# Kernel tuning notes

Measured on AMD Instinct MI355X. Metric: run time of the kernel, lower is better.

Reference implementation:

```python
import jax, jax.numpy as jnp
import numpy as np

D_MODEL, N_HEADS, WINDOW, N_STATE = 1024, 16, 256, 128
B, T = 2, 2048
EPS = 1e-5


def _layernorm(x, g, b):
    mu = jnp.mean(x, axis=-1, keepdims=True)
    var = jnp.mean((x - mu) ** 2, axis=-1, keepdims=True)
    return (x - mu) * jax.lax.rsqrt(var + EPS) * g + b


def setup_inputs() -> dict:
    key = jax.random.key(0)
    ks = jax.random.split(key, 20)
    d, h = D_MODEL, 4 * D_MODEL
    s = lambda k, *shape: jax.random.normal(k, shape, jnp.float32) * 0.02
    return {
        "x": jax.random.normal(ks[0], (B, T, d), jnp.float32),
        "ssm_state": jnp.zeros((B, N_STATE), jnp.float32),
        "ln1_g": jnp.ones((d,), jnp.float32), "ln1_b": jnp.zeros((d,), jnp.float32),
        "wq": s(ks[1], d, d), "bq": jnp.zeros((d,), jnp.float32),
        "wk": s(ks[2], d, d), "bk": jnp.zeros((d,), jnp.float32),
        "wv": s(ks[3], d, d), "bv": jnp.zeros((d,), jnp.float32),
        "wo": s(ks[4], d, d), "bo": jnp.zeros((d,), jnp.float32),
        "wg": s(ks[5], d, d), "bg": jnp.zeros((d,), jnp.float32),
        "A": jax.random.uniform(ks[6], (N_STATE,), jnp.float32, -0.1, 0.1),
        "Bw": s(ks[7], d, N_STATE),
        "Cw": s(ks[8], N_STATE, d),
        "ln2_g": jnp.ones((d,), jnp.float32), "ln2_b": jnp.zeros((d,), jnp.float32),
        "w1": s(ks[9], d, h), "b1": jnp.zeros((h,), jnp.float32),
        "w2": s(ks[10], h, d), "b2": jnp.zeros((d,), jnp.float32),
    }


def _forward(x, ssm_state, ln1_g, ln1_b, wq, bq, wk, bk, wv, bv, wo, bo,
             wg, bg, A, Bw, Cw, ln2_g, ln2_b, w1, b1, w2, b2):
    Bsz, Tlen, d = x.shape
    d_h = d // N_HEADS
    xn = _layernorm(x, ln1_g, ln1_b)

    # --- windowed causal attention (dense, per original) ---
    def heads(y):
        return y.reshape(Bsz, Tlen, N_HEADS, d_h).transpose(0, 2, 1, 3)
    Q = heads(xn @ wq + bq)
    K = heads(xn @ wk + bk)
    V = heads(xn @ wv + bv)
    scores = jnp.einsum("bhqd,bhkd->bhqk", Q, K) / (d_h ** 0.5)
    i = jnp.arange(Tlen)[:, None]
    j = jnp.arange(Tlen)[None, :]
    allowed = (j <= i) & (i - j < WINDOW)
    scores = jnp.where(allowed, scores, -jnp.inf)
    attn = jax.nn.softmax(scores, axis=-1)
    ao = jnp.einsum("bhqk,bhkd->bhqd", attn, V)
    ao = ao.transpose(0, 2, 1, 3).reshape(Bsz, Tlen, d)
    attn_out = ao @ wo + bo

    # --- diagonal SSM scan ---
    u = xn @ Bw  # (B,T,N)
    def step(s, u_t):
        s = A * s + u_t
        return s, s
    new_state, states = jax.lax.scan(step, ssm_state, u.transpose(1, 0, 2))
    ssm_out = states.transpose(1, 0, 2) @ Cw  # (B,T,d)

    # --- gated fusion + residual + MLP ---
    g = jax.nn.sigmoid(xn @ wg + bg)
    x = x + g * attn_out + (1.0 - g) * ssm_out
    xn2 = _layernorm(x, ln2_g, ln2_b)
    mlp = jax.nn.gelu(xn2 @ w1 + b1, approximate=False) @ w2 + b2
    return x + mlp, new_state


def reference(x, ssm_state, ln1_g, ln1_b, wq, bq, wk, bk, wv, bv, wo, bo,
              wg, bg, A, Bw, Cw, ln2_g, ln2_b, w1, b1, w2, b2):
    return _forward(x, ssm_state, ln1_g, ln1_b, wq, bq, wk, bk, wv, bv, wo, bo,
                    wg, bg, A, Bw, Cw, ln2_g, ln2_b, w1, b1, w2, b2)
```

## Files before the change

### kernel.cpp

```cpp
#include <hip/hip_runtime.h>

typedef __attribute__((ext_vector_type(8))) short bf16x8;
typedef __attribute__((ext_vector_type(4))) float f32x4;

#define D_MODEL 1024
#define T_LEN 2048
#define BATCH 2
#define N_HEADS 16
#define D_HEAD 64
#define WINDOW 256
#define N_STATE 128
#define D_FF 4096
#define N_CAT 4224
#define LDQ 4352
#define M_ROWS 4096

static __device__ __forceinline__ float bf2f(unsigned short u) {
  union { unsigned int i; float f; } v; v.i = ((unsigned int)u) << 16; return v.f;
}
static __device__ __forceinline__ unsigned short f2bf(float f) {
  unsigned int x = __float_as_uint(f);
  return (unsigned short)((x + 0x7FFFu + ((x >> 16) & 1u)) >> 16);
}

static __device__ __forceinline__ void gl_lds16(const void* g, void* l) {
  __builtin_amdgcn_global_load_lds(
      (const __attribute__((address_space(1))) unsigned int*)g,
      (__attribute__((address_space(3))) unsigned int*)l, 16, 0, 0);
}

__global__ __launch_bounds__(256) void prep_kernel(
    const float* __restrict__ wq, const float* __restrict__ wk,
    const float* __restrict__ wv, const float* __restrict__ wg,
    const float* __restrict__ wo, const float* __restrict__ Bw,
    const float* __restrict__ Cw, const float* __restrict__ w1,
    const float* __restrict__ w2,
    const float* __restrict__ bq, const float* __restrict__ bk,
    const float* __restrict__ bv, const float* __restrict__ bg,
    unsigned short* __restrict__ WcatT, unsigned short* __restrict__ woT,
    unsigned short* __restrict__ CwT, unsigned short* __restrict__ w1T,
    unsigned short* __restrict__ w2T, float* __restrict__ bcat)
{
  const int bid = blockIdx.x;
  if (bid >= 13568) {
    const int i = (bid - 13568) * 256 + threadIdx.x;
    if (i < LDQ) {
      float v = 0.0f;
      if (i < 1024)      v = bq[i];
      else if (i < 2048) v = bk[i - 1024];
      else if (i < 3072) v = bv[i - 2048];
      else if (i < 4096) v = bg[i - 3072];
      bcat[i] = v;
    }
    return;
  }
  const float* src; unsigned short* dst;
  int N, n_off, ldd, x, y;
  if (bid < 5120) {
    const int z = bid >> 10, t = bid & 1023;
    x = t & 31; y = t >> 5;
    src = (z == 0) ? wq : (z == 1) ? wk : (z == 2) ? wv : (z == 3) ? wg : wo;
    dst = (z < 4) ? WcatT : woT;
    n_off = (z < 4) ? z * 1024 : 0;
    N = 1024; ldd = 1024;
  } else if (bid < 5248) {
    const int t = bid - 5120; x = t & 31; y = t >> 5;
    src = Bw; dst = WcatT; n_off = 4096; N = 128; ldd = 1024;
  } else if (bid < 5376) {
    const int t = bid - 5248; x = t & 3; y = t >> 2;
    src = Cw; dst = CwT; n_off = 0; N = 1024; ldd = 128;
  } else if (bid < 9472) {
    const int t = bid - 5376; x = t & 31; y = t >> 5;
    src = w1; dst = w1T; n_off = 0; N = 4096; ldd = 1024;
  } else {
    const int t = bid - 9472; x = t & 127; y = t >> 7;
    src = w2; dst = w2T; n_off = 0; N = 1024; ldd = 4096;
  }
  __shared__ float tile[32][33];
  const int kt = x * 32, nt = y * 32;
  const int c = threadIdx.x & 31, r0 = threadIdx.x >> 5;
#pragma unroll
  for (int i = 0; i < 4; i++) {
    const int r = r0 + i * 8;
    tile[r][c] = src[(size_t)(kt + r) * N + nt + c];
  }
  __syncthreads();
#pragma unroll
  for (int i = 0; i < 4; i++) {
    const int r = r0 + i * 8;
    dst[(size_t)(n_off + nt + r) * ldd + kt + c] = f2bf(tile[c][r]);
  }
}

__global__ __launch_bounds__(256) void vtrans_kernel(
    const unsigned short* __restrict__ qkvgu, unsigned short* __restrict__ VT)
{
  __shared__ unsigned short tile[32][33];
  const int bh = blockIdx.z;
  const int b = bh >> 4, h = bh & 15;
  const int t0 = blockIdx.x * 32, d0 = blockIdx.y * 32;
  const int c = threadIdx.x & 31, r0 = threadIdx.x >> 5;
#pragma unroll
  for (int i = 0; i < 4; i++) {
    const int r = r0 + i * 8;
    tile[r][c] = qkvgu[((size_t)b * T_LEN + t0 + r) * LDQ + 2048 + h * 64 + d0 + c];
  }
  __syncthreads();
#pragma unroll
  for (int i = 0; i < 4; i++) {
    const int r = r0 + i * 8;
    VT[((size_t)bh * 64 + d0 + r) * T_LEN + t0 + c] = tile[c][r];
  }
}

__global__ __launch_bounds__(256) void ln_kernel(
    const float* __restrict__ x, const float* __restrict__ g,
    const float* __restrict__ b, unsigned short* __restrict__ out)
{
  const int row = blockIdx.x, tid = threadIdx.x;
  const float4 xv = ((const float4*)(x + (size_t)row * 1024))[tid];
  float s  = xv.x + xv.y + xv.z + xv.w;
  float s2 = xv.x * xv.x + xv.y * xv.y + xv.z * xv.z + xv.w * xv.w;
#pragma unroll
  for (int off = 32; off >= 1; off >>= 1) {
    s  += __shfl_down(s, off);
    s2 += __shfl_down(s2, off);
  }
  __shared__ float red[8];
  const int wave = tid >> 6;
  if ((tid & 63) == 0) { red[wave] = s; red[4 + wave] = s2; }
  __syncthreads();
  s  = red[0] + red[1] + red[2] + red[3];
  s2 = red[4] + red[5] + red[6] + red[7];
  const float mu = s * (1.0f / 1024.0f);
  const float rs = rsqrtf(s2 * (1.0f / 1024.0f) - mu * mu + 1e-5f);
  const float4 gv = ((const float4*)g)[tid];
  const float4 bv = ((const float4*)b)[tid];
  ushort4 o;
  o.x = f2bf((xv.x - mu) * rs * gv.x + bv.x);
  o.y = f2bf((xv.y - mu) * rs * gv.y + bv.y);
  o.z = f2bf((xv.z - mu) * rs * gv.z + bv.z);
  o.w = f2bf((xv.w - mu) * rs * gv.w + bv.w);
  ((ushort4*)(out + (size_t)row * 1024))[tid] = o;
}

template<int ACT>
__global__ __launch_bounds__(256, 4) void gemm128ho(
    const unsigned short* __restrict__ A, const unsigned short* __restrict__ BT,
    const float* __restrict__ bias, unsigned short* __restrict__ C,
    int ldc, int K, int nby)
{
  __shared__ char smem[32768];
  char* const As = smem;
  char* const Bs = smem + 16384;
  const int nwg = gridDim.x;
  int bid = blockIdx.x;
  {
    const int q = nwg >> 3, r = nwg & 7, xx = bid & 7, o = bid >> 3;
    bid = (xx < r ? xx * (q + 1) : r * (q + 1) + (xx - r) * q) + o;
  }
  const int per_group = 8 * nby;
  const int grp = bid / per_group, rem = bid % per_group;
  const int m0 = (grp * 8 + (rem & 7)) * 128;
  const int n0 = (rem >> 3) * 128;

  const int tid = threadIdx.x, lane = tid & 63, wave = tid >> 6;
  const int l15 = lane & 15, lg = lane >> 4;
  const int wm = (wave >> 1) * 64, wn = (wave & 1) * 64;
  f32x4 acc[4][4];
#pragma unroll
  for (int i = 0; i < 4; i++)
#pragma unroll
    for (int j = 0; j < 4; j++) acc[i][j] = (f32x4){0.f, 0.f, 0.f, 0.f};

  const char* srcA[4]; const char* srcB[4];
#pragma unroll
  for (int j = 0; j < 4; j++) {
    const int p = j * 4096 + tid * 16;
    const int R = p >> 7;
    const int cb = (p & 127) ^ ((R & 7) << 4);
    srcA[j] = (const char*)A  + (size_t)(m0 + R) * (size_t)(K * 2) + cb;
    srcB[j] = (const char*)BT + (size_t)(n0 + R) * (size_t)(K * 2) + cb;
  }

  const int NT = K >> 6;
  for (int t = 0; t < NT; ++t) {
    __syncthreads();
#pragma unroll
    for (int j = 0; j < 4; j++) {
      gl_lds16(srcA[j] + (size_t)t * 128, As + j * 4096 + tid * 16);
      gl_lds16(srcB[j] + (size_t)t * 128, Bs + j * 4096 + tid * 16);
    }
    __syncthreads();
    bf16x8 af[4][2], bfr[4][2];
#pragma unroll
    for (int mf = 0; mf < 4; mf++)
#pragma unroll
      for (int ks = 0; ks < 2; ks++) {
        const int R = wm + mf * 16 + l15;
        af[mf][ks] = *(const bf16x8*)(As + (R << 7) + ((ks * 64 + lg * 16) ^ ((R & 7) << 4)));
      }
#pragma unroll
    for (int nf = 0; nf < 4; nf++)
#pragma unroll
      for (int ks = 0; ks < 2; ks++) {
        const int R = wn + nf * 16 + l15;
        bfr[nf][ks] = *(const bf16x8*)(Bs + (R << 7) + ((ks * 64 + lg * 16) ^ ((R & 7) << 4)));
      }
#pragma unroll
    for (int mf = 0; mf < 4; mf++)
#pragma unroll
      for (int nf = 0; nf < 4; nf++)
#pragma unroll
        for (int ks = 0; ks < 2; ks++)
          acc[mf][nf] = __builtin_amdgcn_mfma_f32_16x16x32_bf16(
              af[mf][ks], bfr[nf][ks], acc[mf][nf], 0, 0, 0);
  }

  __syncthreads();
  unsigned short (*Ct)[128] = (unsigned short(*)[128])smem;
#pragma unroll
  for (int nf = 0; nf < 4; nf++) {
    const int col = wn + nf * 16 + l15;
    const float bv = bias[n0 + col];
#pragma unroll
    for (int mf = 0; mf < 4; mf++) {
      const int rbase = wm + mf * 16 + lg * 4;
#pragma unroll
      for (int r = 0; r < 4; r++) {
        float v = acc[mf][nf][r] + bv;
        if (ACT == 2) v = 0.5f * v * (1.0f + erff(v * 0.70710678118654752f));
        Ct[rbase + r][col] = f2bf(v);
      }
    }
  }
  __syncthreads();
#pragma unroll
  for (int pass = 0; pass < 8; pass++) {
    const int idx = pass * 256 + tid;
    const int row = idx >> 4, c8 = (idx & 15) * 8;
    const uint4 d = *(const uint4*)&Ct[row][c8];
    *(uint4*)(C + (size_t)(m0 + row) * ldc + n0 + c8) = d;
  }
}

template<int ACT, bool OUT_BF16, bool RESID>
__global__ __launch_bounds__(256, 4) void gemm_ho(
    const unsigned short* __restrict__ A, const unsigned short* __restrict__ BT,
    const float* __restrict__ bias, const float* __restrict__ resid,
    void* __restrict__ Cout, int ldc, int K, int nbx)
{
  __shared__ char As[16384];
  __shared__ char Bs[8192];
  const int nwg = gridDim.x;
  int bid = blockIdx.x;
  {
    const int q = nwg >> 3, r = nwg & 7, xx = bid & 7, o = bid >> 3;
    bid = (xx < r ? xx * (q + 1) : r * (q + 1) + (xx - r) * q) + o;
  }
  const int m0 = (bid % nbx) * 128;
  const int n0 = (bid / nbx) * 64;
  const int tid = threadIdx.x, lane = tid & 63, wave = tid >> 6;
  const int l15 = lane & 15, lg = lane >> 4;
  const int wm = (wave & 1) * 64, wn = (wave >> 1) * 32;
  f32x4 acc[4][2];
#pragma unroll
  for (int i = 0; i < 4; i++)
#pragma unroll
    for (int j = 0; j < 2; j++) acc[i][j] = (f32x4){0.f, 0.f, 0.f, 0.f};

  const char* srcA[4]; const char* srcB[2];
#pragma unroll
  for (int j = 0; j < 4; j++) {
    const int p = j * 4096 + tid * 16;
    const int R = p >> 7;
    const int cb = (p & 127) ^ ((R & 7) << 4);
    srcA[j] = (const char*)A + (size_t)(m0 + R) * (size_t)(K * 2) + cb;
    if (j < 2) srcB[j] = (const char*)BT + (size_t)(n0 + R) * (size_t)(K * 2) + cb;
  }

  const int NT = K >> 6;
  for (int t = 0; t < NT; ++t) {
    __syncthreads();
#pragma unroll
    for (int j = 0; j < 4; j++)
      gl_lds16(srcA[j] + (size_t)t * 128, As + j * 4096 + tid * 16);
#pragma unroll
    for (int j = 0; j < 2; j++)
      gl_lds16(srcB[j] + (size_t)t * 128, Bs + j * 4096 + tid * 16);
    __syncthreads();
    bf16x8 af[4][2], bfr[2][2];
#pragma unroll
    for (int mf = 0; mf < 4; mf++)
#pragma unroll
      for (int ks = 0; ks < 2; ks++) {
        const int R = wm + mf * 16 + l15;
        af[mf][ks] = *(const bf16x8*)(As + (R << 7) + ((ks * 64 + lg * 16) ^ ((R & 7) << 4)));
      }
#pragma unroll
    for (int nf = 0; nf < 2; nf++)
#pragma unroll
      for (int ks = 0; ks < 2; ks++) {
        const int R = wn + nf * 16 + l15;
        bfr[nf][ks] = *(const bf16x8*)(Bs + (R << 7) + ((ks * 64 + lg * 16) ^ ((R & 7) << 4)));
      }
#pragma unroll
    for (int mf = 0; mf < 4; mf++)
#pragma unroll
      for (int nf = 0; nf < 2; nf++)
#pragma unroll
        for (int ks = 0; ks < 2; ks++)
          acc[mf][nf] = __builtin_amdgcn_mfma_f32_16x16x32_bf16(
              af[mf][ks], bfr[nf][ks], acc[mf][nf], 0, 0, 0);
  }

  if (OUT_BF16) {
    __syncthreads();
    unsigned short (*Ct)[64] = (unsigned short(*)[64])As;
#pragma unroll
    for (int nf = 0; nf < 2; nf++) {
      const int col = wn + nf * 16 + l15;
      const float bv = bias ? bias[n0 + col] : 0.0f;
#pragma unroll
      for (int mf = 0; mf < 4; mf++) {
        const int rbase = wm + mf * 16 + lg * 4;
#pragma unroll
        for (int r = 0; r < 4; r++) {
          float v = acc[mf][nf][r] + bv;
          if (ACT == 2) v = 0.5f * v * (1.0f + erff(v * 0.70710678118654752f));
          Ct[rbase + r][col] = f2bf(v);
        }
      }
    }
    __syncthreads();
    unsigned short* Cb = (unsigned short*)Cout;
#pragma unroll
    for (int pass = 0; pass < 4; pass++) {
      const int idx = pass * 256 + tid;
      const int row = idx >> 3, c8 = (idx & 7) * 8;
      const uint4 d = *(const uint4*)&Ct[row][c8];
      *(uint4*)(Cb + (size_t)(m0 + row) * ldc + n0 + c8) = d;
    }
  } else {
#pragma unroll
    for (int nf = 0; nf < 2; nf++) {
      const int col = n0 + wn + nf * 16 + l15;
      const float bv = bias ? bias[col] : 0.0f;
#pragma unroll
      for (int mf = 0; mf < 4; mf++) {
        const int rbase = m0 + wm + mf * 16 + lg * 4;
#pragma unroll
        for (int r = 0; r < 4; r++) {
          float v = acc[mf][nf][r] + bv;
          if (ACT == 2) v = 0.5f * v * (1.0f + erff(v * 0.70710678118654752f));
          const size_t idx = (size_t)(rbase + r) * ldc + col;
          if (RESID) v += resid[idx];
          ((float*)Cout)[idx] = v;
        }
      }
    }
  }
}

__global__ __launch_bounds__(256, 4) void gemm_dual(
    const unsigned short* __restrict__ A1, const unsigned short* __restrict__ BT1,
    const float* __restrict__ bias1, unsigned short* __restrict__ C1, int K1,
    const unsigned short* __restrict__ A2, const unsigned short* __restrict__ BT2,
    const float* __restrict__ bias2, unsigned short* __restrict__ C2, int K2)
{
  __shared__ char As[16384];
  __shared__ char Bs[8192];
  const int nwg = gridDim.x;
  int bid = blockIdx.x;
  {
    const int q = nwg >> 3, r = nwg & 7, xx = bid & 7, o = bid >> 3;
    bid = (xx < r ? xx * (q + 1) : r * (q + 1) + (xx - r) * q) + o;
  }
  const int job = bid >> 9;
  const int inner = bid & 511;
  const unsigned short* A  = job ? A2 : A1;
  const unsigned short* BT = job ? BT2 : BT1;
  const float* bias        = job ? bias2 : bias1;
  unsigned short* C        = job ? C2 : C1;
  const int K              = job ? K2 : K1;
  const int m0 = (inner & 31) * 128;
  const int n0 = (inner >> 5) * 64;
  const int ldc = 1024;

  const int tid = threadIdx.x, lane = tid & 63, wave = tid >> 6;
  const int l15 = lane & 15, lg = lane >> 4;
  const int wm = (wave & 1) * 64, wn = (wave >> 1) * 32;
  f32x4 acc[4][2];
#pragma unroll
  for (int i = 0; i < 4; i++)
#pragma unroll
    for (int j = 0; j < 2; j++) acc[i][j] = (f32x4){0.f, 0.f, 0.f, 0.f};

  const char* srcA[4]; const char* srcB[2];
#pragma unroll
  for (int j = 0; j < 4; j++) {
    const int p = j * 4096 + tid * 16;
    const int R = p >> 7;
    const int cb = (p & 127) ^ ((R & 7) << 4);
    srcA[j] = (const char*)A + (size_t)(m0 + R) * (size_t)(K * 2) + cb;
    if (j < 2) srcB[j] = (const char*)BT + (size_t)(n0 + R) * (size_t)(K * 2) + cb;
  }

  const int NT = K >> 6;
  for (int t = 0; t < NT; ++t) {
    __syncthreads();
#pragma unroll
    for (int j = 0; j < 4; j++)
      gl_lds16(srcA[j] + (size_t)t * 128, As + j * 4096 + tid * 16);
#pragma unroll
    for (int j = 0; j < 2; j++)
      gl_lds16(srcB[j] + (size_t)t * 128, Bs + j * 4096 + tid * 16);
    __syncthreads();
    bf16x8 af[4][2], bfr[2][2];
#pragma unroll
    for (int mf = 0; mf < 4; mf++)
#pragma unroll
      for (int ks = 0; ks < 2; ks++) {
        const int R = wm + mf * 16 + l15;
        af[mf][ks] = *(const bf16x8*)(As + (R << 7) + ((ks * 64 + lg * 16) ^ ((R & 7) << 4)));
      }
#pragma unroll
    for (int nf = 0; nf < 2; nf++)
#pragma unroll
      for (int ks = 0; ks < 2; ks++) {
        const int R = wn + nf * 16 + l15;
        bfr[nf][ks] = *(const bf16x8*)(Bs + (R << 7) + ((ks * 64 + lg * 16) ^ ((R & 7) << 4)));
      }
#pragma unroll
    for (int mf = 0; mf < 4; mf++)
#pragma unroll
      for (int nf = 0; nf < 2; nf++)
#pragma unroll
        for (int ks = 0; ks < 2; ks++)
          acc[mf][nf] = __builtin_amdgcn_mfma_f32_16x16x32_bf16(
              af[mf][ks], bfr[nf][ks], acc[mf][nf], 0, 0, 0);
  }

  __syncthreads();
  unsigned short (*Ct)[64] = (unsigned short(*)[64])As;
#pragma unroll
  for (int nf = 0; nf < 2; nf++) {
    const int col = wn + nf * 16 + l15;
    const float bv = bias ? bias[n0 + col] : 0.0f;
#pragma unroll
    for (int mf = 0; mf < 4; mf++) {
      const int rbase = wm + mf * 16 + lg * 4;
#pragma unroll
      for (int r = 0; r < 4; r++)
        Ct[rbase + r][col] = f2bf(acc[mf][nf][r] + bv);
    }
  }
  __syncthreads();
#pragma unroll
  for (int pass = 0; pass < 4; pass++) {
    const int idx = pass * 256 + tid;
    const int row = idx >> 3, c8 = (idx & 7) * 8;
    const uint4 d = *(const uint4*)&Ct[row][c8];
    *(uint4*)(C + (size_t)(m0 + row) * ldc + n0 + c8) = d;
  }
}

__global__ __launch_bounds__(256) void attn_scan_kernel(
    const unsigned short* __restrict__ qkvgu, const unsigned short* __restrict__ VT,
    unsigned short* __restrict__ ao, const float* __restrict__ Avec,
    const float* __restrict__ s0, unsigned short* __restrict__ states,
    float* __restrict__ out_state)
{
  __shared__ float S[16][276];
  const int tid = threadIdx.x;

  if (blockIdx.x >= 128) {
    if (blockIdx.y != 0 || blockIdx.z != 0 || blockIdx.x > 129) return;
    float (*finals)[128] = (float(*)[128])&S[0][0];
    const int b = blockIdx.x - 128;
    const int c = tid >> 6;
    const int n0 = (tid & 63) * 2;
    const float a0 = Avec[n0], a1 = Avec[n0 + 1];
    float sv0 = (c == 0) ? s0[b * 128 + n0]     : 0.0f;
    float sv1 = (c == 0) ? s0[b * 128 + n0 + 1] : 0.0f;
    const size_t ubase = (size_t)b * T_LEN * LDQ + 4096 + n0;
    unsigned short* sp = states + (size_t)b * T_LEN * N_STATE + n0;
    const int t0 = c * 512;
#pragma unroll 8
    for (int t = t0; t < t0 + 512; t++) {
      const ushort2 u = *(const ushort2*)&qkvgu[ubase + (size_t)t * LDQ];
      sv0 = fmaf(a0, sv0, bf2f(u.x));
      sv1 = fmaf(a1, sv1, bf2f(u.y));
      ushort2 o; o.x = f2bf(sv0); o.y = f2bf(sv1);
      *(ushort2*)&sp[(size_t)t * N_STATE] = o;
    }
    finals[c][n0] = sv0;
    finals[c][n0 + 1] = sv1;
    if (c == 3) { out_state[b * 128 + n0] = sv0; out_state[b * 128 + n0 + 1] = sv1; }
    __syncthreads();
    if (c > 0) {
      const float c0 = finals[c - 1][n0];
      const float c1 = finals[c - 1][n0 + 1];
      float f0 = a0, f1 = a1;
      for (int t = t0; t < t0 + 512; t++) {
        if (f0 == 0.0f && f1 == 0.0f) break;
        ushort2 cur = *(ushort2*)&sp[(size_t)t * N_STATE];
        cur.x = f2bf(bf2f(cur.x) + f0 * c0);
        cur.y = f2bf(bf2f(cur.y) + f1 * c1);
        *(ushort2*)&sp[(size_t)t * N_STATE] = cur;
        f0 *= a0; f1 *= a1;
      }
    }
    return;
  }

  unsigned short* P = (unsigned short*)&S[0][0];
  const int bx = ((blockIdx.x & 7) << 4) | (blockIdx.x >> 3);
  const int q0 = bx * 16;
  const int h  = blockIdx.y;
  const int b  = blockIdx.z;
  const int lane = tid & 63, wave = tid >> 6;
  const int l15 = lane & 15, lg = lane >> 4;
  const size_t rowbase = (size_t)b * T_LEN;

  {
    const unsigned short* qp = qkvgu + (rowbase + q0 + l15) * LDQ + h * 64 + lg * 8;
    const bf16x8 aq0 = *(const bf16x8*)qp;
    const bf16x8 aq1 = *(const bf16x8*)(qp + 32);
    for (int kt = wave; kt < 17; kt += 4) {
      const int kbase = q0 - 256 + kt * 16;
      const int krow = kbase + l15;
      const int krc = krow < 0 ? 0 : krow;
      const unsigned short* kp = qkvgu + (rowbase + krc) * LDQ + 1024 + h * 64 + lg * 8;
      const bf16x8 bk0 = *(const bf16x8*)kp;
      const bf16x8 bk1 = *(const bf16x8*)(kp + 32);
      f32x4 sacc = (f32x4){0.f, 0.f, 0.f, 0.f};
      sacc = __builtin_amdgcn_mfma_f32_16x16x32_bf16(aq0, bk0, sacc, 0, 0, 0);
      sacc = __builtin_amdgcn_mfma_f32_16x16x32_bf16(aq1, bk1, sacc, 0, 0, 0);
#pragma unroll
      for (int r = 0; r < 4; r++) {
        const int qi = q0 + lg * 4 + r;
        const int kj = kbase + l15;
        const bool ok = (kj >= 0) && (kj <= qi) && (qi - kj < WINDOW);
        S[lg * 4 + r][kt * 16 + l15] = ok ? sacc[r] * 0.125f : -1e30f;
      }
    }
  }
  __syncthreads();

  {
    const int q = tid >> 4, sub = tid & 15;
    float mx = -1e30f;
    for (int c = sub; c < 272; c += 16) mx = fmaxf(mx, S[q][c]);
#pragma unroll
    for (int off = 8; off >= 1; off >>= 1) mx = fmaxf(mx, __shfl_xor(mx, off));
    float sum = 0.f;
    for (int c = sub; c < 272; c += 16) sum += __expf(S[q][c] - mx);
#pragma unroll
    for (int off = 8; off >= 1; off >>= 1) sum += __shfl_xor(sum, off);
    const float inv = 1.0f / sum;
    unsigned short* Prow = P + q * 552;
    for (int c = sub; c < 288; c += 16) {
      const float pv = (c < 272) ? __expf(S[q][c] - mx) * inv : 0.0f;
      Prow[c] = f2bf(pv);
    }
  }
  __syncthreads();

  {
    f32x4 oacc = (f32x4){0.f, 0.f, 0.f, 0.f};
    const int dn = wave * 16 + l15;
    const unsigned short* vrow = VT + ((size_t)(b * 16 + h) * 64 + dn) * T_LEN;
#pragma unroll
    for (int ks = 0; ks < 9; ks++) {
      const bf16x8 pa = *(const bf16x8*)(P + l15 * 552 + ks * 32 + lg * 8);
      int t = q0 - 256 + ks * 32 + lg * 8;
      t = t < 0 ? 0 : (t > T_LEN - 8 ? T_LEN - 8 : t);
      const bf16x8 vb = *(const bf16x8*)(vrow + t);
      oacc = __builtin_amdgcn_mfma_f32_16x16x32_bf16(pa, vb, oacc, 0, 0, 0);
    }
#pragma unroll
    for (int r = 0; r < 4; r++)
      ao[(rowbase + q0 + lg * 4 + r) * D_MODEL + h * 64 + dn] = f2bf(oacc[r]);
  }
}

__global__ __launch_bounds__(256) void fusion_ln2_kernel(
    const float* __restrict__ x, const unsigned short* __restrict__ qkvgu,
    const unsigned short* __restrict__ attn, const unsigned short* __restrict__ ssm,
    const float* __restrict__ g2, const float* __restrict__ b2,
    float* __restrict__ out, unsigned short* __restrict__ xn2)
{
  const int row = blockIdx.x, tid = threadIdx.x;
  const size_t e4 = (size_t)row * 1024 + tid * 4;
  const float4 xv = *(const float4*)(x + e4);
  const ushort4 au = *(const ushort4*)(attn + e4);
  const ushort4 su = *(const ushort4*)(ssm + e4);
  const ushort4 gu = *(const ushort4*)(qkvgu + (size_t)row * LDQ + 3072 + tid * 4);
  float4 o;
  {
    const float ga = 1.0f / (1.0f + __expf(-bf2f(gu.x)));
    const float gb = 1.0f / (1.0f + __expf(-bf2f(gu.y)));
    const float gc = 1.0f / (1.0f + __expf(-bf2f(gu.z)));
    const float gd = 1.0f / (1.0f + __expf(-bf2f(gu.w)));
    o.x = xv.x + ga * bf2f(au.x) + (1.0f - ga) * bf2f(su.x);
    o.y = xv.y + gb * bf2f(au.y) + (1.0f - gb) * bf2f(su.y);
    o.z = xv.z + gc * bf2f(au.z) + (1.0f - gc) * bf2f(su.z);
    o.w = xv.w + gd * bf2f(au.w) + (1.0f - gd) * bf2f(su.w);
  }
  *(float4*)(out + e4) = o;

  float s  = o.x + o.y + o.z + o.w;
  float s2 = o.x * o.x + o.y * o.y + o.z * o.z + o.w * o.w;
#pragma unroll
  for (int off = 32; off >= 1; off >>= 1) {
    s  += __shfl_down(s, off);
    s2 += __shfl_down(s2, off);
  }
  __shared__ float red[8];
  const int wave = tid >> 6;
  if ((tid & 63) == 0) { red[wave] = s; red[4 + wave] = s2; }
  __syncthreads();
  s  = red[0] + red[1] + red[2] + red[3];
  s2 = red[4] + red[5] + red[6] + red[7];
  const float mu = s * (1.0f / 1024.0f);
  const float rs = rsqrtf(s2 * (1.0f / 1024.0f) - mu * mu + 1e-5f);
  const float4 gv = ((const float4*)g2)[tid];
  const float4 bv = ((const float4*)b2)[tid];
  ushort4 ov;
  ov.x = f2bf((o.x - mu) * rs * gv.x + bv.x);
  ov.y = f2bf((o.y - mu) * rs * gv.y + bv.y);
  ov.z = f2bf((o.z - mu) * rs * gv.z + bv.z);
  ov.w = f2bf((o.w - mu) * rs * gv.w + bv.w);
  ((ushort4*)(xn2 + (size_t)row * 1024))[tid] = ov;
}

extern "C" void kernel_launch(void* const* d_in, const int* in_sizes, int n_in,
                              void* d_out, int out_size, void* d_ws, size_t ws_size,
                              hipStream_t stream)
{
  const float* x     = (const float*)d_in[0];
  const float* ssm0  = (const float*)d_in[1];
  const float* ln1_g = (const float*)d_in[2];
  const float* ln1_b = (const float*)d_in[3];
  const float* wq    = (const float*)d_in[4];
  const float* bq    = (const float*)d_in[5];
  const float* wk    = (const float*)d_in[6];
  const float* bk    = (const float*)d_in[7];
  const float* wv    = (const float*)d_in[8];
  const float* bv    = (const float*)d_in[9];
  const float* wo    = (const float*)d_in[10];
  const float* bo    = (const float*)d_in[11];
  const float* wg    = (const float*)d_in[12];
  const float* bg    = (const float*)d_in[13];
  const float* Av    = (const float*)d_in[14];
  const float* Bw    = (const float*)d_in[15];
  const float* Cw    = (const float*)d_in[16];
  const float* ln2_g = (const float*)d_in[17];
  const float* ln2_b = (const float*)d_in[18];
  const float* w1    = (const float*)d_in[19];
  const float* b1    = (const float*)d_in[20];
  const float* w2    = (const float*)d_in[21];
  const float* b2    = (const float*)d_in[22];

  char* p = (char*)d_ws;
  auto take = [&](size_t bytes) { char* q = p; p += (bytes + 255) & ~(size_t)255; return q; };
  unsigned short* WcatT  = (unsigned short*)take((size_t)LDQ * 1024 * 2);
  unsigned short* woT    = (unsigned short*)take((size_t)1024 * 1024 * 2);
  unsigned short* CwT    = (unsigned short*)take((size_t)1024 * 128 * 2);
  unsigned short* w1T    = (unsigned short*)take((size_t)4096 * 1024 * 2);
  unsigned short* w2T    = (unsigned short*)take((size_t)1024 * 4096 * 2);
  float*          bcat   = (float*)take((size_t)LDQ * 4);
  unsigned short* xn     = (unsigned short*)take((size_t)M_ROWS * 1024 * 2);
  unsigned short* qkvgu  = (unsigned short*)take((size_t)M_ROWS * LDQ * 2);
  unsigned short* VT     = (unsigned short*)take((size_t)BATCH * N_HEADS * 64 * T_LEN * 2);
  unsigned short* ao     = (unsigned short*)take((size_t)M_ROWS * 1024 * 2);
  unsigned short* states = (unsigned short*)take((size_t)M_ROWS * N_STATE * 2);
  unsigned short* attn_o = (unsigned short*)take((size_t)M_ROWS * 1024 * 2);
  unsigned short* ssm_o  = (unsigned short*)take((size_t)M_ROWS * 1024 * 2);
  unsigned short* hbuf   = qkvgu;

  float* outx = (float*)d_out;
  float* out_state = outx + (size_t)M_ROWS * 1024;

  prep_kernel<<<13585, 256, 0, stream>>>(
      wq, wk, wv, wg, wo, Bw, Cw, w1, w2, bq, bk, bv, bg,
      WcatT, woT, CwT, w1T, w2T, bcat);

  ln_kernel<<<M_ROWS, 256, 0, stream>>>(x, ln1_g, ln1_b, xn);
  gemm128ho<0><<<32 * 34, 256, 0, stream>>>(xn, WcatT, bcat, qkvgu, LDQ, 1024, 34);
  vtrans_kernel<<<dim3(64, 2, 32), 256, 0, stream>>>(qkvgu, VT);
  attn_scan_kernel<<<dim3(130, 16, 2), 256, 0, stream>>>(
      qkvgu, VT, ao, Av, ssm0, states, out_state);
  gemm_dual<<<1024, 256, 0, stream>>>(
      ao, woT, bo, attn_o, 1024,
      states, CwT, nullptr, ssm_o, 128);
  fusion_ln2_kernel<<<4096, 256, 0, stream>>>(
      x, qkvgu, attn_o, ssm_o, ln2_g, ln2_b, outx, xn);
  gemm128ho<2><<<32 * 32, 256, 0, stream>>>(xn, w1T, b1, hbuf, 4096, 1024, 32);
  gemm_ho<0, false, true><<<32 * 16, 256, 0, stream>>>(
      hbuf, w2T, b2, outx, outx, 1024, 4096, 32);
}
```

Before: 296.4 us.

## Process 32 queries per attention block to halve per-block K/V overhead

The windowed attention block now covers 32 query rows instead of 16, with waves split into two query tiles and two key/head-dim halves. The 288-wide key window is shared across both query tiles, so K and V rows are loaded once per 32 queries instead of once per 16, and the grid halves. Shared memory grows to a 32x308 score buffer, and launch bounds request 4 blocks per CU. Fewer, larger blocks may reduce parallelism, and the attention stage is only part of the total runtime.

```diff
diff --git a/kernel.cpp b/kernel.cpp
--- a/kernel.cpp
+++ b/kernel.cpp
@@ -465,19 +465,19 @@
   }
 }
 
-__global__ __launch_bounds__(256) void attn_scan_kernel(
+__global__ __launch_bounds__(256, 4) void attn_scan_kernel(
     const unsigned short* __restrict__ qkvgu, const unsigned short* __restrict__ VT,
     unsigned short* __restrict__ ao, const float* __restrict__ Avec,
     const float* __restrict__ s0, unsigned short* __restrict__ states,
     float* __restrict__ out_state)
 {
-  __shared__ float S[16][276];
+  __shared__ float S[32][308];
   const int tid = threadIdx.x;
 
-  if (blockIdx.x >= 128) {
-    if (blockIdx.y != 0 || blockIdx.z != 0 || blockIdx.x > 129) return;
+  if (blockIdx.x >= 64) {
+    if (blockIdx.y != 0 || blockIdx.z != 0 || blockIdx.x > 65) return;
     float (*finals)[128] = (float(*)[128])&S[0][0];
-    const int b = blockIdx.x - 128;
+    const int b = blockIdx.x - 64;
     const int c = tid >> 6;
     const int n0 = (tid & 63) * 2;
     const float a0 = Avec[n0], a1 = Avec[n0 + 1];
@@ -515,20 +515,22 @@
   }
 
   unsigned short* P = (unsigned short*)&S[0][0];
-  const int bx = ((blockIdx.x & 7) << 4) | (blockIdx.x >> 3);
-  const int q0 = bx * 16;
+  const int bx = ((blockIdx.x & 7) << 3) | (blockIdx.x >> 3);
+  const int q0 = bx * 32;
   const int h  = blockIdx.y;
   const int b  = blockIdx.z;
   const int lane = tid & 63, wave = tid >> 6;
   const int l15 = lane & 15, lg = lane >> 4;
+  const int qt = wave & 1;
+  const int kstart = q0 - 256;
   const size_t rowbase = (size_t)b * T_LEN;
 
   {
-    const unsigned short* qp = qkvgu + (rowbase + q0 + l15) * LDQ + h * 64 + lg * 8;
+    const unsigned short* qp = qkvgu + (rowbase + q0 + qt * 16 + l15) * LDQ + h * 64 + lg * 8;
     const bf16x8 aq0 = *(const bf16x8*)qp;
     const bf16x8 aq1 = *(const bf16x8*)(qp + 32);
-    for (int kt = wave; kt < 17; kt += 4) {
-      const int kbase = q0 - 256 + kt * 16;
+    for (int kt = (wave >> 1); kt < 18; kt += 2) {
+      const int kbase = kstart + kt * 16;
       const int krow = kbase + l15;
       const int krc = krow < 0 ? 0 : krow;
       const unsigned short* kp = qkvgu + (rowbase + krc) * LDQ + 1024 + h * 64 + lg * 8;
@@ -539,49 +541,51 @@
       sacc = __builtin_amdgcn_mfma_f32_16x16x32_bf16(aq1, bk1, sacc, 0, 0, 0);
 #pragma unroll
       for (int r = 0; r < 4; r++) {
-        const int qi = q0 + lg * 4 + r;
+        const int qi = q0 + qt * 16 + lg * 4 + r;
         const int kj = kbase + l15;
         const bool ok = (kj >= 0) && (kj <= qi) && (qi - kj < WINDOW);
-        S[lg * 4 + r][kt * 16 + l15] = ok ? sacc[r] * 0.125f : -1e30f;
+        S[qt * 16 + lg * 4 + r][kt * 16 + l15] = ok ? sacc[r] * 0.125f : -1e30f;
       }
     }
   }
   __syncthreads();
 
   {
-    const int q = tid >> 4, sub = tid & 15;
+    const int row = tid >> 3, sub = tid & 7;
     float mx = -1e30f;
-    for (int c = sub; c < 272; c += 16) mx = fmaxf(mx, S[q][c]);
-#pragma unroll
-    for (int off = 8; off >= 1; off >>= 1) mx = fmaxf(mx, __shfl_xor(mx, off));
+    for (int c = sub; c < 288; c += 8) mx = fmaxf(mx, S[row][c]);
+#pragma unroll
+    for (int off = 4; off >= 1; off >>= 1) mx = fmaxf(mx, __shfl_xor(mx, off));
     float sum = 0.f;
-    for (int c = sub; c < 272; c += 16) sum += __expf(S[q][c] - mx);
-#pragma unroll
-    for (int off = 8; off >= 1; off >>= 1) sum += __shfl_xor(sum, off);
+    for (int c = sub; c < 288; c += 8) sum += __expf(S[row][c] - mx);
+#pragma unroll
+    for (int off = 4; off >= 1; off >>= 1) sum += __shfl_xor(sum, off);
     const float inv = 1.0f / sum;
-    unsigned short* Prow = P + q * 552;
-    for (int c = sub; c < 288; c += 16) {
-      const float pv = (c < 272) ? __expf(S[q][c] - mx) * inv : 0.0f;
-      Prow[c] = f2bf(pv);
-    }
+    unsigned short* Prow = P + row * 616;
+    for (int c = sub; c < 288; c += 8)
+      Prow[c] = f2bf(__expf(S[row][c] - mx) * inv);
   }
   __syncthreads();
 
   {
-    f32x4 oacc = (f32x4){0.f, 0.f, 0.f, 0.f};
-    const int dn = wave * 16 + l15;
-    const unsigned short* vrow = VT + ((size_t)(b * 16 + h) * 64 + dn) * T_LEN;
-#pragma unroll
-    for (int ks = 0; ks < 9; ks++) {
-      const bf16x8 pa = *(const bf16x8*)(P + l15 * 552 + ks * 32 + lg * 8);
-      int t = q0 - 256 + ks * 32 + lg * 8;
-      t = t < 0 ? 0 : (t > T_LEN - 8 ? T_LEN - 8 : t);
-      const bf16x8 vb = *(const bf16x8*)(vrow + t);
-      oacc = __builtin_amdgcn_mfma_f32_16x16x32_bf16(pa, vb, oacc, 0, 0, 0);
-    }
-#pragma unroll
-    for (int r = 0; r < 4; r++)
-      ao[(rowbase + q0 + lg * 4 + r) * D_MODEL + h * 64 + dn] = f2bf(oacc[r]);
+    const int dt0 = (wave >> 1) * 2;
+#pragma unroll
+    for (int j = 0; j < 2; j++) {
+      const int dn = (dt0 + j) * 16 + l15;
+      const unsigned short* vrow = VT + ((size_t)(b * 16 + h) * 64 + dn) * T_LEN;
+      f32x4 oacc = (f32x4){0.f, 0.f, 0.f, 0.f};
+#pragma unroll
+      for (int ks = 0; ks < 9; ks++) {
+        const bf16x8 pa = *(const bf16x8*)(P + (qt * 16 + l15) * 616 + ks * 32 + lg * 8);
+        int t = kstart + ks * 32 + lg * 8;
+        t = t < 0 ? 0 : (t > T_LEN - 8 ? T_LEN - 8 : t);
+        const bf16x8 vb = *(const bf16x8*)(vrow + t);
+        oacc = __builtin_amdgcn_mfma_f32_16x16x32_bf16(pa, vb, oacc, 0, 0, 0);
+      }
+#pragma unroll
+      for (int r = 0; r < 4; r++)
+        ao[(rowbase + q0 + qt * 16 + lg * 4 + r) * D_MODEL + h * 64 + dn] = f2bf(oacc[r]);
+    }
   }
 }
 
@@ -690,7 +694,7 @@
   ln_kernel<<<M_ROWS, 256, 0, stream>>>(x, ln1_g, ln1_b, xn);
   gemm128ho<0><<<32 * 34, 256, 0, stream>>>(xn, WcatT, bcat, qkvgu, LDQ, 1024, 34);
   vtrans_kernel<<<dim3(64, 2, 32), 256, 0, stream>>>(qkvgu, VT);
-  attn_scan_kernel<<<dim3(130, 16, 2), 256, 0, stream>>>(
+  attn_scan_kernel<<<dim3(66, 16, 2), 256, 0, stream>>>(
       qkvgu, VT, ao, Av, ssm0, states, out_state);
   gemm_dual<<<1024, 256, 0, stream>>>(
       ao, woT, bo, attn_o, 1024,
```

Result: no change. 293.0 us (-1.2%).
